# Kernel tuning notes

Hardware: AMD Instinct MI355X
Metric: run time of the kernel (lower is better)

Reference implementation:

```python
import jax, jax.numpy as jnp
import numpy as np

B = 1024      # graphs per batch
N = 64        # nodes per graph
DEG = 8       # edges per node
E = B * N * DEG
V = 52737     # vocab (different_ids)
D = 512       # embed / hidden dim
K1, K2, K3 = 52, 42, 34  # ceil(0.8*64), ceil(0.8*52), ceil(0.8*42)


def setup_inputs() -> dict:
    key = jax.random.key(0)
    ks = jax.random.split(key, 40)
    x_ids = jax.random.randint(ks[0], (B * N,), 0, V)
    off = jnp.repeat(jnp.arange(B) * N, N * DEG)  # graph offsets per edge
    edge_src = jax.random.randint(ks[1], (E,), 0, N) + off
    edge_dst = jax.random.randint(ks[2], (E,), 0, N) + off

    def lin(k, i, o):
        return jax.random.normal(k, (i, o), jnp.float32) / np.float32(np.sqrt(i))

    inp = dict(x_ids=x_ids, edge_src=edge_src, edge_dst=edge_dst)
    inp['emb'] = jax.random.normal(ks[3], (V, D), jnp.float32)
    # SAGEConv params: w*l/b*l act on aggregated neighbors, w*r on root
    for i, (kl, kr) in enumerate([(4, 5), (6, 7), (8, 9)], start=1):
        inp[f'w{i}l'] = lin(ks[kl], D, D)
        inp[f'b{i}l'] = jnp.zeros((D,), jnp.float32)
        inp[f'w{i}r'] = lin(ks[kr], D, D)
    # TopKPooling score vectors
    inp['p1'] = jax.random.normal(ks[10], (D,), jnp.float32)
    inp['p2'] = jax.random.normal(ks[11], (D,), jnp.float32)
    inp['p3'] = jax.random.normal(ks[12], (D,), jnp.float32)
    dims = [(1024, 512), (512, 256), (256, 128), (128, 64), (64, 1)]
    for i, (di, do) in enumerate(dims, start=1):
        inp[f'lw{i}'] = lin(ks[12 + i], di, do)
        inp[f'lb{i}'] = jnp.zeros((do,), jnp.float32)
    return inp


def _sage(x, src, dst, emask, wl, bl, wr):
    # PyG SAGEConv: mean-aggregate neighbor messages (src -> dst), plus root term
    n = x.shape[0]
    msg = x[src] * emask[:, None]
    s = jax.ops.segment_sum(msg, dst, num_segments=n)
    c = jax.ops.segment_sum(emask, dst, num_segments=n)
    agg = s / jnp.maximum(c, 1.0)[:, None]  # empty neighborhoods -> 0
    return agg @ wl + bl + x @ wr


def _topk_pool(x, src, dst, emask, w, k):
    # PyG TopKPooling: score = tanh(x.w / ||w||); keep top-k per graph, gate x
    n = x.shape[0]
    n_per = n // B
    score = jnp.tanh((x @ w) / jnp.linalg.norm(w))
    _, idx = jax.lax.top_k(score.reshape(B, n_per), k)      # [B, k] local ids
    perm = (idx + jnp.arange(B)[:, None] * n_per).reshape(-1)  # global ids
    x_new = x[perm] * score[perm][:, None]
    new_id = jnp.full((n,), -1, jnp.int32).at[perm].set(jnp.arange(B * k, dtype=jnp.int32))
    ns, nd = new_id[src], new_id[dst]
    valid = emask * (ns >= 0) * (nd >= 0)
    ns = jnp.where(valid > 0, ns, 0)
    nd = jnp.where(valid > 0, nd, 0)
    return x_new, ns, nd, valid.astype(x.dtype)


def _readout(x, k):
    xg = x.reshape(B, k, -1)
    return jnp.concatenate([xg.max(axis=1), xg.mean(axis=1)], axis=1)  # [B, 2F]


def _forward(x_ids, edge_src, edge_dst, emb,
             w1l, b1l, w1r, w2l, b2l, w2r, w3l, b3l, w3r,
             p1, p2, p3,
             lw1, lb1, lw2, lb2, lw3, lb3, lw4, lb4, lw5, lb5):
    x = emb[x_ids]                                  # [B*N, D]
    src, dst = edge_src, edge_dst
    emask = jnp.ones((E,), x.dtype)

    x = jax.nn.relu(_sage(x, src, dst, emask, w1l, b1l, w1r))
    x, src, dst, emask = _topk_pool(x, src, dst, emask, p1, K1)
    x1 = _readout(x, K1)

    x = jax.nn.relu(_sage(x, src, dst, emask, w2l, b2l, w2r))
    x, src, dst, emask = _topk_pool(x, src, dst, emask, p2, K2)
    x2 = _readout(x, K2)

    x = jax.nn.relu(_sage(x, src, dst, emask, w3l, b3l, w3r))
    x, src, dst, emask = _topk_pool(x, src, dst, emask, p3, K3)
    x3 = _readout(x, K3)

    h = x1 + x2 + x3                                # [B, 1024]
    h = jax.nn.relu(h @ lw1 + lb1)
    h = jax.nn.relu(h @ lw2 + lb2)
    h = jax.nn.relu(h @ lw3 + lb3)
    h = jax.nn.relu(h @ lw4 + lb4)
    # dropout p=0.5 is identity in eval mode
    return jax.nn.sigmoid(h @ lw5 + lb5)[:, 0]      # [B]


def reference(x_ids, edge_src, edge_dst, emb,
              w1l, b1l, w1r, w2l, b2l, w2r, w3l, b3l, w3r,
              p1, p2, p3,
              lw1, lb1, lw2, lb2, lw3, lb3, lw4, lb4, lw5, lb5):
    return _forward(x_ids, edge_src, edge_dst, emb,
                    w1l, b1l, w1r, w2l, b2l, w2r, w3l, b3l, w3r,
                    p1, p2, p3,
                    lw1, lb1, lw2, lb2, lw3, lb3, lw4, lb4, lw5, lb5)
```

## Files before the change

### kernel.cpp

```cpp
#include <hip/hip_runtime.h>
#include <math.h>

#define BG 1024
#define EPG 512
#define ETOT (BG*EPG)
#define DIM 512
#define KP1 52
#define KP2 42
#define KP3 34

typedef unsigned int uint;
typedef short s16x8 __attribute__((ext_vector_type(8)));
typedef float f32x4 __attribute__((ext_vector_type(4)));

__device__ __forceinline__ unsigned short f2b(float x) {
    uint u = __float_as_uint(x);
    u = u + 0x7fffu + ((u >> 16) & 1u);
    return (unsigned short)(u >> 16);
}
__device__ __forceinline__ float b2f(unsigned short h) {
    return __uint_as_float(((uint)h) << 16);
}
__device__ __forceinline__ void splitf(float x, unsigned short& h, unsigned short& l) {
    h = f2b(x);
    l = f2b(x - b2f(h));
}
__device__ __forceinline__ uint pk2(unsigned short a, unsigned short b) {
    return (uint)a | ((uint)b << 16);
}

__device__ __forceinline__ void gload16(const void* g, void* l) {
    __builtin_amdgcn_global_load_lds(
        (const __attribute__((address_space(1))) void*)g,
        (__attribute__((address_space(3))) void*)l, 16, 0, 0);
}

__global__ void __launch_bounds__(256)
gather_split(const int* __restrict__ ids, const float* __restrict__ emb,
             unsigned short* __restrict__ Xhi, unsigned short* __restrict__ Xlo)
{
    int tid = blockIdx.x * 256 + threadIdx.x;
    int row = tid >> 6;
    int c8  = (tid & 63) * 8;
    const float4* s = (const float4*)(emb + (size_t)ids[row] * DIM + c8);
    float4 v0 = s[0], v1 = s[1];
    float vs[8] = {v0.x,v0.y,v0.z,v0.w,v1.x,v1.y,v1.z,v1.w};
    unsigned short h[8], l[8];
#pragma unroll
    for (int i = 0; i < 8; ++i) splitf(vs[i], h[i], l[i]);
    uint4 H, L;
    H.x = pk2(h[0],h[1]); H.y = pk2(h[2],h[3]); H.z = pk2(h[4],h[5]); H.w = pk2(h[6],h[7]);
    L.x = pk2(l[0],l[1]); L.y = pk2(l[2],l[3]); L.z = pk2(l[4],l[5]); L.w = pk2(l[6],l[7]);
    *(uint4*)(Xhi + (size_t)row * DIM + c8) = H;
    *(uint4*)(Xlo + (size_t)row * DIM + c8) = L;
}

struct WPtrs { const float* w[6]; };

__global__ void __launch_bounds__(256)
split_wT_all(WPtrs p, unsigned short* __restrict__ WT)
{
    const int wi = blockIdx.x >> 8;
    const int bb = blockIdx.x & 255;
    const float* W = p.w[wi];
    unsigned short* Thi = WT + (size_t)(2 * wi) * DIM * DIM;
    unsigned short* Tlo = Thi + (size_t)DIM * DIM;
    __shared__ float tl[32][33];
    const int t  = threadIdx.x;
    const int bx = bb & 15;
    const int by = bb >> 4;
    const int lx = t & 31, ly = t >> 5;
    for (int r = ly; r < 32; r += 8)
        tl[r][lx] = W[(size_t)(by*32 + r) * DIM + bx*32 + lx];
    __syncthreads();
    for (int r = ly; r < 32; r += 8) {
        float v = tl[lx][r];
        unsigned short h, l; splitf(v, h, l);
        size_t o = (size_t)(bx*32 + r) * DIM + by*32 + lx;
        Thi[o] = h; Tlo[o] = l;
    }
}

template<int NPER>
__global__ void __launch_bounds__(256, 4)
agg_lds4(const unsigned short* __restrict__ Xhi, const unsigned short* __restrict__ Xlo,
         const int* __restrict__ esrc, const int* __restrict__ edst,
         const float* __restrict__ emask,
         unsigned short* __restrict__ Ghi, unsigned short* __restrict__ Glo)
{
    const int g  = blockIdx.x >> 2;
    const int c0 = (blockIdx.x & 3) * 128;
    const int t  = threadIdx.x;
    __shared__ __align__(16) unsigned short xs[NPER * 256];
    __shared__ int ldst[EPG];
    __shared__ int lsrc[EPG];
    __shared__ int ssrc[EPG];
    __shared__ int cnt4[4][64];
    __shared__ int offs[NPER + 1];

    for (int s = t; s < NPER * 32; s += 256) {
        const int row  = s >> 5;
        const int half = (s >> 4) & 1;
        const int c8   = (s & 15) * 8;
        const unsigned short* src =
            (half ? Xlo : Xhi) + (size_t)(g * NPER + row) * DIM + c0 + c8;
        gload16(src, (char*)xs + (size_t)s * 16);
    }
    const int eb = g * EPG;
    for (int e = t; e < EPG; e += 256) {
        float m = emask ? emask[eb + e] : 1.0f;
        ldst[e] = (m > 0.f) ? (edst[eb + e] - g * NPER) : -1;
        lsrc[e] = esrc[eb + e] - g * NPER;
    }
    __syncthreads();
    {
        const int d = t & 63, q = t >> 6;
        int c = 0;
        for (int e = q * 128; e < q * 128 + 128; ++e) c += (ldst[e] == d);
        cnt4[q][d] = c;
    }
    __syncthreads();
    if (t == 0) {
        int s = 0;
        for (int i = 0; i < NPER; ++i) {
            offs[i] = s;
            s += cnt4[0][i] + cnt4[1][i] + cnt4[2][i] + cnt4[3][i];
        }
        offs[NPER] = s;
    }
    __syncthreads();
    {
        const int d = t & 63, q = t >> 6;
        if (d < NPER) {
            int w = offs[d];
            for (int q2 = 0; q2 < q; ++q2) w += cnt4[q2][d];
            for (int e = q * 128; e < q * 128 + 128; ++e)
                if (ldst[e] == d) ssrc[w++] = lsrc[e];
        }
    }
    __syncthreads();
    const int ch = (t & 31) * 4;
    const int d0 = t >> 5;
    for (int d = d0; d < NPER; d += 8) {
        const int cA = offs[d], cB = offs[d + 1];
        float s0 = 0.f, s1 = 0.f, s2 = 0.f, s3 = 0.f;
        for (int j = cA; j < cB; ++j) {
            const int base = ssrc[j] * 256 + ch;
            ushort4 h = *(const ushort4*)&xs[base];
            ushort4 l = *(const ushort4*)&xs[base + 128];
            s0 += b2f(h.x) + b2f(l.x);
            s1 += b2f(h.y) + b2f(l.y);
            s2 += b2f(h.z) + b2f(l.z);
            s3 += b2f(h.w) + b2f(l.w);
        }
        const float den = fmaxf((float)(cB - cA), 1.0f);
        s0 /= den; s1 /= den; s2 /= den; s3 /= den;
        unsigned short h0,h1,h2,h3,l0,l1,l2,l3;
        splitf(s0,h0,l0); splitf(s1,h1,l1); splitf(s2,h2,l2); splitf(s3,h3,l3);
        const size_t wo = (size_t)(g * NPER + d) * DIM + c0 + ch;
        *(uint2*)(Ghi + wo) = make_uint2(pk2(h0,h1), pk2(h2,h3));
        *(uint2*)(Glo + wo) = make_uint2(pk2(l0,l1), pk2(l2,l3));
    }
}

__global__ void __launch_bounds__(256)
gemm_sage(const unsigned short* __restrict__ Ghi, const unsigned short* __restrict__ Glo,
          const unsigned short* __restrict__ WLhi, const unsigned short* __restrict__ WLlo,
          const unsigned short* __restrict__ Xhi, const unsigned short* __restrict__ Xlo,
          const unsigned short* __restrict__ WRhi, const unsigned short* __restrict__ WRlo,
          const float* __restrict__ bias, float* __restrict__ C, int M)
{
    __shared__ unsigned short sA[128 * 64];
    __shared__ unsigned short sW[128 * 64];

    const int t = threadIdx.x;
    const uint nwg = gridDim.x;
    const uint q8  = nwg >> 3;
    const uint bid = blockIdx.x;
    const uint sw  = (bid & 7) * q8 + (bid >> 3);
    const int  m0  = (int)(sw >> 2) * 128;
    const int  n0  = (int)(sw & 3) * 128;

    const int l  = t & 63;
    const int w  = t >> 6;
    const int wr = w >> 1;
    const int wc = w & 1;
    const int lr = l & 15;
    const int lq = l >> 4;

    f32x4 acc[4][4];
#pragma unroll
    for (int i = 0; i < 4; ++i)
#pragma unroll
        for (int j = 0; j < 4; ++j) acc[i][j] = (f32x4){0.f, 0.f, 0.f, 0.f};

    uint srow[4], soff[4];
#pragma unroll
    for (int i = 0; i < 4; ++i) {
        uint p = (uint)i * 256u + (uint)t;
        uint row = p >> 3, pc = p & 7;
        srow[i] = row;
        soff[i] = (pc ^ (row & 7u)) * 8u;
    }

#pragma unroll 1
    for (int s = 0; s < 6; ++s) {
        const int src = (s >= 3) ? 1 : 0;
        const int combo = s - src * 3;
        const unsigned short* Ap = src ? ((combo == 2) ? Xlo : Xhi)
                                       : ((combo == 2) ? Glo : Ghi);
        const unsigned short* Wp = src ? ((combo == 1) ? WRlo : WRhi)
                                       : ((combo == 1) ? WLlo : WLhi);
#pragma unroll 1
        for (int kt = 0; kt < 8; ++kt) {
            const int kb = kt * 64;
#pragma unroll
            for (int i = 0; i < 4; ++i) {
                const unsigned short* ga =
                    Ap + (size_t)(m0 + srow[i]) * DIM + kb + soff[i];
                const unsigned short* gw =
                    Wp + (size_t)(n0 + srow[i]) * DIM + kb + soff[i];
                uint p16 = ((uint)i * 256u + (uint)t) * 16u;
                gload16(ga, (char*)sA + p16);
                gload16(gw, (char*)sW + p16);
            }
            __syncthreads();
#pragma unroll
            for (int ks = 0; ks < 2; ++ks) {
                s16x8 af[4], wf[4];
#pragma unroll
                for (int i = 0; i < 4; ++i) {
                    int arow = wr * 64 + i * 16 + lr;
                    int off = arow * 128 + 16 * ((ks * 4 + lq) ^ (arow & 7));
                    af[i] = *(const s16x8*)((const char*)sA + off);
                }
#pragma unroll
                for (int j = 0; j < 4; ++j) {
                    int wrow = wc * 64 + j * 16 + lr;
                    int off = wrow * 128 + 16 * ((ks * 4 + lq) ^ (wrow & 7));
                    wf[j] = *(const s16x8*)((const char*)sW + off);
                }
#pragma unroll
                for (int i = 0; i < 4; ++i)
#pragma unroll
                    for (int j = 0; j < 4; ++j)
                        acc[i][j] = __builtin_amdgcn_mfma_f32_16x16x32_bf16(
                            af[i], wf[j], acc[i][j], 0, 0, 0);
            }
            __syncthreads();
        }
    }

#pragma unroll
    for (int i = 0; i < 4; ++i) {
        const int r0 = m0 + wr * 64 + i * 16 + lq * 4;
#pragma unroll
        for (int j = 0; j < 4; ++j) {
            const int cc = n0 + wc * 64 + j * 16 + lr;
            const float bv = bias[cc];
#pragma unroll
            for (int r = 0; r < 4; ++r) {
                float v = acc[i][j][r] + bv;
                C[(size_t)(r0 + r) * DIM + cc] = fmaxf(v, 0.f);
            }
        }
    }
}

template<int NPER, int KEEP>
__global__ void __launch_bounds__(256)
topk_split(const float* __restrict__ Y, const float* __restrict__ p,
           unsigned short* __restrict__ Xhi, unsigned short* __restrict__ Xlo,
           int* __restrict__ newid)
{
    const int g = blockIdx.x;
    const int t = threadIdx.x;
    const int wave = t >> 6, lane = t & 63;
    __shared__ float ssc[NPER];
    __shared__ float spnorm;
    __shared__ int   perm[KEEP];
    __shared__ float sgate[KEEP];

    if (wave == 0) {
        float v = 0.f;
#pragma unroll
        for (int i = 0; i < 8; ++i) { float x = p[lane + i * 64]; v = fmaf(x, x, v); }
#pragma unroll
        for (int off = 32; off; off >>= 1) v += __shfl_down(v, off);
        if (lane == 0) spnorm = sqrtf(v);
    }
    for (int nl = wave; nl < NPER; nl += 4) {
        const float* yr = Y + (size_t)(g * NPER + nl) * DIM;
        float v = 0.f;
#pragma unroll
        for (int i = 0; i < 8; ++i) v = fmaf(yr[lane + i * 64], p[lane + i * 64], v);
#pragma unroll
        for (int off = 32; off; off >>= 1) v += __shfl_down(v, off);
        if (lane == 0) ssc[nl] = v;
    }
    __syncthreads();
    float s = 0.f;
    if (t < NPER) s = tanhf(ssc[t] / spnorm);
    __syncthreads();
    if (t < NPER) ssc[t] = s;
    __syncthreads();
    if (t < NPER) {
        int r = 0;
        for (int j = 0; j < NPER; ++j) {
            float sj = ssc[j];
            r += (sj > s) || (sj == s && j < t);
        }
        newid[g * NPER + t] = (r < KEEP) ? (g * KEEP + r) : -1;
        if (r < KEEP) { perm[r] = t; sgate[r] = s; }
    }
    __syncthreads();
    for (int r = 0; r < KEEP; ++r) {
        const float2* src = (const float2*)(Y + (size_t)(g * NPER + perm[r]) * DIM);
        const float sv = sgate[r];
        float2 v = src[t];
        float a = v.x * sv, b = v.y * sv;
        unsigned short ha, la, hb, lb;
        splitf(a, ha, la); splitf(b, hb, lb);
        size_t o = (size_t)(g * KEEP + r) * DIM + 2 * t;
        *(uint*)(Xhi + o) = pk2(ha, hb);
        *(uint*)(Xlo + o) = pk2(la, lb);
    }
}

__global__ void __launch_bounds__(256)
remap_kernel(const int* __restrict__ es, const int* __restrict__ ed,
             const float* __restrict__ em, const int* __restrict__ newid,
             int* __restrict__ nes, int* __restrict__ ned, float* __restrict__ nem)
{
    int e = blockIdx.x * 256 + threadIdx.x;
    if (e >= ETOT) return;
    float m = em ? em[e] : 1.f;
    int s = newid[es[e]];
    int d = newid[ed[e]];
    bool v = (m > 0.f) && (s >= 0) && (d >= 0);
    nes[e] = v ? s : 0;
    ned[e] = v ? d : 0;
    nem[e] = v ? 1.f : 0.f;
}

__global__ void __launch_bounds__(256)
readout_split(const unsigned short* __restrict__ Xhi, const unsigned short* __restrict__ Xlo,
              float* __restrict__ H, int keep, int init)
{
    const int g = blockIdx.x;
    const int t = threadIdx.x;
    for (int c = t; c < DIM; c += 256) {
        float mx = -1e30f, sm = 0.f;
        for (int r = 0; r < keep; ++r) {
            size_t o = (size_t)(g * keep + r) * DIM + c;
            float v = b2f(Xhi[o]) + b2f(Xlo[o]);
            mx = fmaxf(mx, v); sm += v;
        }
        float mean = sm / (float)keep;
        size_t o = (size_t)g * 1024;
        if (init) { H[o + c] = mx;  H[o + 512 + c] = mean; }
        else      { H[o + c] += mx; H[o + 512 + c] += mean; }
    }
}

__global__ void __launch_bounds__(256)
mlp_fused(const float* __restrict__ H,
          const float* __restrict__ lw1, const float* __restrict__ lb1,
          const float* __restrict__ lw2, const float* __restrict__ lb2,
          const float* __restrict__ lw3, const float* __restrict__ lb3,
          const float* __restrict__ lw4, const float* __restrict__ lb4,
          const float* __restrict__ lw5, const float* __restrict__ lb5,
          float* __restrict__ out)
{
    __shared__ float h0[2][1024];
    __shared__ float y1[2][512];
    __shared__ float y2[2][256];
    __shared__ float y3[2][128];
    __shared__ float y4[2][64];
    const int t = threadIdx.x;
    const int r0 = blockIdx.x * 2;

    {
        float4 a = *(const float4*)&H[(size_t)r0 * 1024 + t * 4];
        float4 b = *(const float4*)&H[(size_t)(r0 + 1) * 1024 + t * 4];
        *(float4*)&h0[0][t * 4] = a;
        *(float4*)&h0[1][t * 4] = b;
    }
    __syncthreads();
    {
        float a00 = 0.f, a01 = 0.f, a10 = 0.f, a11 = 0.f;
        const int c = t * 2;
#pragma unroll 4
        for (int k = 0; k < 1024; ++k) {
            float2 wv = *(const float2*)&lw1[(size_t)k * 512 + c];
            float x0 = h0[0][k], x1 = h0[1][k];
            a00 = fmaf(x0, wv.x, a00); a01 = fmaf(x0, wv.y, a01);
            a10 = fmaf(x1, wv.x, a10); a11 = fmaf(x1, wv.y, a11);
        }
        y1[0][c]     = fmaxf(a00 + lb1[c], 0.f);
        y1[0][c + 1] = fmaxf(a01 + lb1[c + 1], 0.f);
        y1[1][c]     = fmaxf(a10 + lb1[c], 0.f);
        y1[1][c + 1] = fmaxf(a11 + lb1[c + 1], 0.f);
    }
    __syncthreads();
    {
        float a0 = 0.f, a1 = 0.f;
#pragma unroll 4
        for (int k = 0; k < 512; ++k) {
            float wv = lw2[(size_t)k * 256 + t];
            a0 = fmaf(y1[0][k], wv, a0);
            a1 = fmaf(y1[1][k], wv, a1);
        }
        y2[0][t] = fmaxf(a0 + lb2[t], 0.f);
        y2[1][t] = fmaxf(a1 + lb2[t], 0.f);
    }
    __syncthreads();
    if (t < 128) {
        float a0 = 0.f, a1 = 0.f;
#pragma unroll 4
        for (int k = 0; k < 256; ++k) {
            float wv = lw3[(size_t)k * 128 + t];
            a0 = fmaf(y2[0][k], wv, a0);
            a1 = fmaf(y2[1][k], wv, a1);
        }
        y3[0][t] = fmaxf(a0 + lb3[t], 0.f);
        y3[1][t] = fmaxf(a1 + lb3[t], 0.f);
    }
    __syncthreads();
    if (t < 64) {
        float a0 = 0.f, a1 = 0.f;
#pragma unroll 4
        for (int k = 0; k < 128; ++k) {
            float wv = lw4[(size_t)k * 64 + t];
            a0 = fmaf(y3[0][k], wv, a0);
            a1 = fmaf(y3[1][k], wv, a1);
        }
        y4[0][t] = fmaxf(a0 + lb4[t], 0.f);
        y4[1][t] = fmaxf(a1 + lb4[t], 0.f);
    }
    __syncthreads();
    const int wv = t >> 6, ln = t & 63;
    if (wv < 2) {
        float v = y4[wv][ln] * lw5[ln];
#pragma unroll
        for (int off = 32; off; off >>= 1) v += __shfl_down(v, off);
        if (ln == 0) out[r0 + wv] = 1.f / (1.f + expf(-(v + lb5[0])));
    }
}

extern "C" void kernel_launch(void* const* d_in, const int* in_sizes, int n_in,
                              void* d_out, int out_size, void* d_ws, size_t ws_size,
                              hipStream_t stream)
{
    const int*   x_ids = (const int*)d_in[0];
    const int*   esrc  = (const int*)d_in[1];
    const int*   edst  = (const int*)d_in[2];
    const float* emb   = (const float*)d_in[3];
    const float* w1l = (const float*)d_in[4],  *b1l = (const float*)d_in[5],  *w1r = (const float*)d_in[6];
    const float* w2l = (const float*)d_in[7],  *b2l = (const float*)d_in[8],  *w2r = (const float*)d_in[9];
    const float* w3l = (const float*)d_in[10], *b3l = (const float*)d_in[11], *w3r = (const float*)d_in[12];
    const float* p1  = (const float*)d_in[13];
    const float* p2  = (const float*)d_in[14];
    const float* p3  = (const float*)d_in[15];
    const float* lw1 = (const float*)d_in[16], *lb1 = (const float*)d_in[17];
    const float* lw2 = (const float*)d_in[18], *lb2 = (const float*)d_in[19];
    const float* lw3 = (const float*)d_in[20], *lb3 = (const float*)d_in[21];
    const float* lw4 = (const float*)d_in[22], *lb4 = (const float*)d_in[23];
    const float* lw5 = (const float*)d_in[24], *lb5 = (const float*)d_in[25];
    float* out = (float*)d_out;

    const size_t PL = (size_t)65536 * DIM;
    unsigned short* Xhi = (unsigned short*)d_ws;
    unsigned short* Xlo = Xhi + PL;
    unsigned short* Ghi = Xlo + PL;
    unsigned short* Glo = Ghi + PL;
    float* Cc = (float*)(Glo + PL);
    float* H  = Cc + PL;
    int* newid = (int*)(H + (size_t)1024 * 1024);
    int*   ES2 = newid + 65536;
    int*   ED2 = ES2 + ETOT;
    float* EM2 = (float*)(ED2 + ETOT);
    int*   ES3 = (int*)(EM2 + ETOT);
    int*   ED3 = ES3 + ETOT;
    float* EM3 = (float*)(ED3 + ETOT);
    unsigned short* WT = (unsigned short*)(EM3 + ETOT);
    const size_t WSZ = (size_t)DIM * DIM;
    unsigned short *w1lh = WT + 0*WSZ,  *w1ll = WT + 1*WSZ;
    unsigned short *w1rh = WT + 2*WSZ,  *w1rl = WT + 3*WSZ;
    unsigned short *w2lh = WT + 4*WSZ,  *w2ll = WT + 5*WSZ;
    unsigned short *w2rh = WT + 6*WSZ,  *w2rl = WT + 7*WSZ;
    unsigned short *w3lh = WT + 8*WSZ,  *w3ll = WT + 9*WSZ;
    unsigned short *w3rh = WT + 10*WSZ, *w3rl = WT + 11*WSZ;

    WPtrs wp;
    wp.w[0] = w1l; wp.w[1] = w1r; wp.w[2] = w2l;
    wp.w[3] = w2r; wp.w[4] = w3l; wp.w[5] = w3r;
    split_wT_all<<<6 * 256, 256, 0, stream>>>(wp, WT);

    gather_split<<<16384, 256, 0, stream>>>(x_ids, emb, Xhi, Xlo);
    agg_lds4<64><<<BG * 4, 256, 0, stream>>>(Xhi, Xlo, esrc, edst, nullptr, Ghi, Glo);
    gemm_sage<<<(65536/128)*4, 256, 0, stream>>>(Ghi, Glo, w1lh, w1ll,
                                                 Xhi, Xlo, w1rh, w1rl, b1l, Cc, 65536);
    topk_split<64, KP1><<<BG, 256, 0, stream>>>(Cc, p1, Xhi, Xlo, newid);
    remap_kernel<<<ETOT/256, 256, 0, stream>>>(esrc, edst, nullptr, newid, ES2, ED2, EM2);
    readout_split<<<BG, 256, 0, stream>>>(Xhi, Xlo, H, KP1, 1);

    agg_lds4<KP1><<<BG * 4, 256, 0, stream>>>(Xhi, Xlo, ES2, ED2, EM2, Ghi, Glo);
    gemm_sage<<<(53248/128)*4, 256, 0, stream>>>(Ghi, Glo, w2lh, w2ll,
                                                 Xhi, Xlo, w2rh, w2rl, b2l, Cc, 53248);
    topk_split<KP1, KP2><<<BG, 256, 0, stream>>>(Cc, p2, Xhi, Xlo, newid);
    remap_kernel<<<ETOT/256, 256, 0, stream>>>(ES2, ED2, EM2, newid, ES3, ED3, EM3);
    readout_split<<<BG, 256, 0, stream>>>(Xhi, Xlo, H, KP2, 0);

    agg_lds4<KP2><<<BG * 4, 256, 0, stream>>>(Xhi, Xlo, ES3, ED3, EM3, Ghi, Glo);
    gemm_sage<<<(43008/128)*4, 256, 0, stream>>>(Ghi, Glo, w3lh, w3ll,
                                                 Xhi, Xlo, w3rh, w3rl, b3l, Cc, 43008);
    topk_split<KP2, KP3><<<BG, 256, 0, stream>>>(Cc, p3, Xhi, Xlo, newid);
    readout_split<<<BG, 256, 0, stream>>>(Xhi, Xlo, H, KP3, 0);

    mlp_fused<<<512, 256, 0, stream>>>(H, lw1, lb1, lw2, lb2, lw3, lb3,
                                       lw4, lb4, lw5, lb5, out);
}
```

Before: 1.389 ms.

## Use 256x256 double-buffered 8-wave GEMM for SAGE layers

Replaces the 128x128, 4-wave SAGE GEMM with a 256x256-tile, 512-thread kernel. The new kernel double-buffers LDS and prefetches the next k-slice while the current one runs MFMAs. All six hi/lo split segments are flattened into one 48-step k loop, and MFMA phases are interleaved with barriers and setprio. The aim is to hide global-load latency and raise operand reuse per tile. The cost is 128KB of LDS and fewer workgroups, which lowers occupancy and gives a poorer tail for the smaller M values (43008 is not divisible by 256*8 swizzle groups, so risk there).

```diff
diff --git a/kernel.cpp b/kernel.cpp
--- a/kernel.cpp
+++ b/kernel.cpp
@@ -163,97 +163,122 @@
     }
 }
 
-__global__ void __launch_bounds__(256)
-gemm_sage(const unsigned short* __restrict__ Ghi, const unsigned short* __restrict__ Glo,
-          const unsigned short* __restrict__ WLhi, const unsigned short* __restrict__ WLlo,
-          const unsigned short* __restrict__ Xhi, const unsigned short* __restrict__ Xlo,
-          const unsigned short* __restrict__ WRhi, const unsigned short* __restrict__ WRlo,
-          const float* __restrict__ bias, float* __restrict__ C, int M)
-{
-    __shared__ unsigned short sA[128 * 64];
-    __shared__ unsigned short sW[128 * 64];
+__global__ void __launch_bounds__(512)
+gemm_sage8(const unsigned short* __restrict__ Ghi, const unsigned short* __restrict__ Glo,
+           const unsigned short* __restrict__ WLhi, const unsigned short* __restrict__ WLlo,
+           const unsigned short* __restrict__ Xhi, const unsigned short* __restrict__ Xlo,
+           const unsigned short* __restrict__ WRhi, const unsigned short* __restrict__ WRlo,
+           const float* __restrict__ bias, float* __restrict__ C, int M)
+{
+    __shared__ unsigned short sA[2][256 * 64];
+    __shared__ unsigned short sW[2][256 * 64];
 
     const int t = threadIdx.x;
     const uint nwg = gridDim.x;
     const uint q8  = nwg >> 3;
     const uint bid = blockIdx.x;
     const uint sw  = (bid & 7) * q8 + (bid >> 3);
-    const int  m0  = (int)(sw >> 2) * 128;
-    const int  n0  = (int)(sw & 3) * 128;
+    const int  m0  = (int)(sw >> 1) * 256;
+    const int  n0  = (int)(sw & 1) * 256;
 
     const int l  = t & 63;
     const int w  = t >> 6;
-    const int wr = w >> 1;
-    const int wc = w & 1;
+    const int wr = w >> 2;
+    const int wc = w & 3;
     const int lr = l & 15;
     const int lq = l >> 4;
 
-    f32x4 acc[4][4];
-#pragma unroll
-    for (int i = 0; i < 4; ++i)
+    f32x4 acc[8][4];
+#pragma unroll
+    for (int i = 0; i < 8; ++i)
 #pragma unroll
         for (int j = 0; j < 4; ++j) acc[i][j] = (f32x4){0.f, 0.f, 0.f, 0.f};
 
     uint srow[4], soff[4];
 #pragma unroll
     for (int i = 0; i < 4; ++i) {
-        uint p = (uint)i * 256u + (uint)t;
-        uint row = p >> 3, pc = p & 7;
-        srow[i] = row;
-        soff[i] = (pc ^ (row & 7u)) * 8u;
-    }
+        uint p = (uint)i * 512u + (uint)t;
+        srow[i] = p >> 3;
+        soff[i] = ((p & 7u) ^ (srow[i] & 7u)) * 8u;
+    }
+
+    const unsigned short* Aseg;
+    const unsigned short* Wseg;
+    int kb;
+#define SEGSEL(kt)                                                     \
+    {   int s_ = (kt) >> 3; kb = ((kt) & 7) << 6;                      \
+        if      (s_ == 0) { Aseg = Ghi; Wseg = WLhi; }                 \
+        else if (s_ == 1) { Aseg = Ghi; Wseg = WLlo; }                 \
+        else if (s_ == 2) { Aseg = Glo; Wseg = WLhi; }                 \
+        else if (s_ == 3) { Aseg = Xhi; Wseg = WRhi; }                 \
+        else if (s_ == 4) { Aseg = Xhi; Wseg = WRlo; }                 \
+        else              { Aseg = Xlo; Wseg = WRhi; } }
+
+#define STAGE(dst)                                                     \
+    _Pragma("unroll")                                                  \
+    for (int i = 0; i < 4; ++i) {                                      \
+        const unsigned short* ga =                                     \
+            Aseg + (size_t)(m0 + (int)srow[i]) * DIM + kb + soff[i];   \
+        const unsigned short* gw =                                     \
+            Wseg + (size_t)(n0 + (int)srow[i]) * DIM + kb + soff[i];   \
+        uint p16 = ((uint)i * 512u + (uint)t) * 16u;                   \
+        gload16(ga, (char*)sA[dst] + p16);                             \
+        gload16(gw, (char*)sW[dst] + p16);                             \
+    }
+
+    SEGSEL(0);
+    STAGE(0);
+    int cur = 0;
 
 #pragma unroll 1
-    for (int s = 0; s < 6; ++s) {
-        const int src = (s >= 3) ? 1 : 0;
-        const int combo = s - src * 3;
-        const unsigned short* Ap = src ? ((combo == 2) ? Xlo : Xhi)
-                                       : ((combo == 2) ? Glo : Ghi);
-        const unsigned short* Wp = src ? ((combo == 1) ? WRlo : WRhi)
-                                       : ((combo == 1) ? WLlo : WLhi);
-#pragma unroll 1
-        for (int kt = 0; kt < 8; ++kt) {
-            const int kb = kt * 64;
-#pragma unroll
-            for (int i = 0; i < 4; ++i) {
-                const unsigned short* ga =
-                    Ap + (size_t)(m0 + srow[i]) * DIM + kb + soff[i];
-                const unsigned short* gw =
-                    Wp + (size_t)(n0 + srow[i]) * DIM + kb + soff[i];
-                uint p16 = ((uint)i * 256u + (uint)t) * 16u;
-                gload16(ga, (char*)sA + p16);
-                gload16(gw, (char*)sW + p16);
+    for (int kt = 0; kt < 48; ++kt) {
+        asm volatile("s_waitcnt vmcnt(0)" ::: "memory");
+        __syncthreads();
+        if (kt < 47) {
+            SEGSEL(kt + 1);
+            STAGE(cur ^ 1);
+        }
+        __builtin_amdgcn_sched_barrier(0);
+        const char* la = (const char*)sA[cur];
+        const char* lw = (const char*)sW[cur];
+#pragma unroll
+        for (int p = 0; p < 4; ++p) {
+            const int ks = p >> 1;
+            const int mh = p & 1;
+            s16x8 af[4], wf[4];
+#pragma unroll
+            for (int i2 = 0; i2 < 4; ++i2) {
+                int arow = wr * 128 + (mh * 4 + i2) * 16 + lr;
+                int off  = arow * 128 + 16 * ((ks * 4 + lq) ^ (arow & 7));
+                af[i2] = *(const s16x8*)(la + off);
             }
+#pragma unroll
+            for (int j = 0; j < 4; ++j) {
+                int wrow = wc * 64 + j * 16 + lr;
+                int off  = wrow * 128 + 16 * ((ks * 4 + lq) ^ (wrow & 7));
+                wf[j] = *(const s16x8*)(lw + off);
+            }
+            __builtin_amdgcn_sched_barrier(0);
             __syncthreads();
-#pragma unroll
-            for (int ks = 0; ks < 2; ++ks) {
-                s16x8 af[4], wf[4];
-#pragma unroll
-                for (int i = 0; i < 4; ++i) {
-                    int arow = wr * 64 + i * 16 + lr;
-                    int off = arow * 128 + 16 * ((ks * 4 + lq) ^ (arow & 7));
-                    af[i] = *(const s16x8*)((const char*)sA + off);
-                }
-#pragma unroll
-                for (int j = 0; j < 4; ++j) {
-                    int wrow = wc * 64 + j * 16 + lr;
-                    int off = wrow * 128 + 16 * ((ks * 4 + lq) ^ (wrow & 7));
-                    wf[j] = *(const s16x8*)((const char*)sW + off);
-                }
-#pragma unroll
-                for (int i = 0; i < 4; ++i)
-#pragma unroll
-                    for (int j = 0; j < 4; ++j)
-                        acc[i][j] = __builtin_amdgcn_mfma_f32_16x16x32_bf16(
-                            af[i], wf[j], acc[i][j], 0, 0, 0);
-            }
+            __builtin_amdgcn_s_setprio(1);
+#pragma unroll
+            for (int i2 = 0; i2 < 4; ++i2)
+#pragma unroll
+                for (int j = 0; j < 4; ++j)
+                    acc[mh * 4 + i2][j] = __builtin_amdgcn_mfma_f32_16x16x32_bf16(
+                        af[i2], wf[j], acc[mh * 4 + i2][j], 0, 0, 0);
+            __builtin_amdgcn_s_setprio(0);
+            __builtin_amdgcn_sched_barrier(0);
             __syncthreads();
         }
-    }
-
-#pragma unroll
-    for (int i = 0; i < 4; ++i) {
-        const int r0 = m0 + wr * 64 + i * 16 + lq * 4;
+        cur ^= 1;
+    }
+#undef STAGE
+#undef SEGSEL
+
+#pragma unroll
+    for (int i = 0; i < 8; ++i) {
+        const int r0 = m0 + wr * 128 + i * 16 + lq * 4;
 #pragma unroll
         for (int j = 0; j < 4; ++j) {
             const int cc = n0 + wc * 64 + j * 16 + lr;
@@ -499,22 +524,22 @@
 
     gather_split<<<16384, 256, 0, stream>>>(x_ids, emb, Xhi, Xlo);
     agg_lds4<64><<<BG * 4, 256, 0, stream>>>(Xhi, Xlo, esrc, edst, nullptr, Ghi, Glo);
-    gemm_sage<<<(65536/128)*4, 256, 0, stream>>>(Ghi, Glo, w1lh, w1ll,
-                                                 Xhi, Xlo, w1rh, w1rl, b1l, Cc, 65536);
+    gemm_sage8<<<(65536/256)*2, 512, 0, stream>>>(Ghi, Glo, w1lh, w1ll,
+                                                  Xhi, Xlo, w1rh, w1rl, b1l, Cc, 65536);
     topk_split<64, KP1><<<BG, 256, 0, stream>>>(Cc, p1, Xhi, Xlo, newid);
     remap_kernel<<<ETOT/256, 256, 0, stream>>>(esrc, edst, nullptr, newid, ES2, ED2, EM2);
     readout_split<<<BG, 256, 0, stream>>>(Xhi, Xlo, H, KP1, 1);
 
     agg_lds4<KP1><<<BG * 4, 256, 0, stream>>>(Xhi, Xlo, ES2, ED2, EM2, Ghi, Glo);
-    gemm_sage<<<(53248/128)*4, 256, 0, stream>>>(Ghi, Glo, w2lh, w2ll,
-                                                 Xhi, Xlo, w2rh, w2rl, b2l, Cc, 53248);
+    gemm_sage8<<<(53248/256)*2, 512, 0, stream>>>(Ghi, Glo, w2lh, w2ll,
+                                                  Xhi, Xlo, w2rh, w2rl, b2l, Cc, 53248);
     topk_split<KP1, KP2><<<BG, 256, 0, stream>>>(Cc, p2, Xhi, Xlo, newid);
     remap_kernel<<<ETOT/256, 256, 0, stream>>>(ES2, ED2, EM2, newid, ES3, ED3, EM3);
     readout_split<<<BG, 256, 0, stream>>>(Xhi, Xlo, H, KP2, 0);
 
     agg_lds4<KP2><<<BG * 4, 256, 0, stream>>>(Xhi, Xlo, ES3, ED3, EM3, Ghi, Glo);
-    gemm_sage<<<(43008/128)*4, 256, 0, stream>>>(Ghi, Glo, w3lh, w3ll,
-                                                 Xhi, Xlo, w3rh, w3rl, b3l, Cc, 43008);
+    gemm_sage8<<<(43008/256)*2, 512, 0, stream>>>(Ghi, Glo, w3lh, w3ll,
+                                                  Xhi, Xlo, w3rh, w3rl, b3l, Cc, 43008);
     topk_split<KP2, KP3><<<BG, 256, 0, stream>>>(Cc, p3, Xhi, Xlo, newid);
     readout_split<<<BG, 256, 0, stream>>>(Xhi, Xlo, H, KP3, 0);
 
```

Measured after the change: 1.685 ms. 1.21x slower.

## Fuse top-k pooling, edge remap and readout into one per-graph kernel

Applied to the files above, without the earlier changes.

The top-k selection kernel now also computes the max/mean readout from the gated values it already holds in registers, and remaps that graph's edges using a shared-memory newid table. This drops two kernel launches per pooling stage, the global newid buffer, and the readout's re-read of the split hi/lo node features. In exchange the per-graph block does more serial work, and readout now uses the unsplit fp32 values instead of the hi+lo reconstruction, which can differ slightly. The remap assumes edge sources and destinations stay inside their own graph.

```diff
diff --git a/kernel.cpp b/kernel.cpp
--- a/kernel.cpp
+++ b/kernel.cpp
@@ -267,11 +267,14 @@
     }
 }
 
-template<int NPER, int KEEP>
+template<int NPER, int KEEP, bool REMAP, bool INIT>
 __global__ void __launch_bounds__(256)
-topk_split(const float* __restrict__ Y, const float* __restrict__ p,
+pool_fused(const float* __restrict__ Y, const float* __restrict__ p,
            unsigned short* __restrict__ Xhi, unsigned short* __restrict__ Xlo,
-           int* __restrict__ newid)
+           const int* __restrict__ es, const int* __restrict__ ed,
+           const float* __restrict__ em,
+           int* __restrict__ nes, int* __restrict__ ned, float* __restrict__ nem,
+           float* __restrict__ H)
 {
     const int g = blockIdx.x;
     const int t = threadIdx.x;
@@ -280,6 +283,7 @@
     __shared__ float spnorm;
     __shared__ int   perm[KEEP];
     __shared__ float sgate[KEEP];
+    __shared__ int   lnewid[NPER];
 
     if (wave == 0) {
         float v = 0.f;
@@ -310,56 +314,50 @@
             float sj = ssc[j];
             r += (sj > s) || (sj == s && j < t);
         }
-        newid[g * NPER + t] = (r < KEEP) ? (g * KEEP + r) : -1;
+        lnewid[t] = (r < KEEP) ? (g * KEEP + r) : -1;
         if (r < KEEP) { perm[r] = t; sgate[r] = s; }
     }
     __syncthreads();
+
+    float mx0 = -1e30f, mx1 = -1e30f, sm0 = 0.f, sm1 = 0.f;
     for (int r = 0; r < KEEP; ++r) {
-        const float2* src = (const float2*)(Y + (size_t)(g * NPER + perm[r]) * DIM);
+        const float2 v = ((const float2*)(Y + (size_t)(g * NPER + perm[r]) * DIM))[t];
         const float sv = sgate[r];
-        float2 v = src[t];
         float a = v.x * sv, b = v.y * sv;
+        mx0 = fmaxf(mx0, a); mx1 = fmaxf(mx1, b);
+        sm0 += a; sm1 += b;
         unsigned short ha, la, hb, lb;
         splitf(a, ha, la); splitf(b, hb, lb);
         size_t o = (size_t)(g * KEEP + r) * DIM + 2 * t;
         *(uint*)(Xhi + o) = pk2(ha, hb);
         *(uint*)(Xlo + o) = pk2(la, lb);
     }
-}
-
-__global__ void __launch_bounds__(256)
-remap_kernel(const int* __restrict__ es, const int* __restrict__ ed,
-             const float* __restrict__ em, const int* __restrict__ newid,
-             int* __restrict__ nes, int* __restrict__ ned, float* __restrict__ nem)
-{
-    int e = blockIdx.x * 256 + threadIdx.x;
-    if (e >= ETOT) return;
-    float m = em ? em[e] : 1.f;
-    int s = newid[es[e]];
-    int d = newid[ed[e]];
-    bool v = (m > 0.f) && (s >= 0) && (d >= 0);
-    nes[e] = v ? s : 0;
-    ned[e] = v ? d : 0;
-    nem[e] = v ? 1.f : 0.f;
-}
-
-__global__ void __launch_bounds__(256)
-readout_split(const unsigned short* __restrict__ Xhi, const unsigned short* __restrict__ Xlo,
-              float* __restrict__ H, int keep, int init)
-{
-    const int g = blockIdx.x;
-    const int t = threadIdx.x;
-    for (int c = t; c < DIM; c += 256) {
-        float mx = -1e30f, sm = 0.f;
-        for (int r = 0; r < keep; ++r) {
-            size_t o = (size_t)(g * keep + r) * DIM + c;
-            float v = b2f(Xhi[o]) + b2f(Xlo[o]);
-            mx = fmaxf(mx, v); sm += v;
-        }
-        float mean = sm / (float)keep;
-        size_t o = (size_t)g * 1024;
-        if (init) { H[o + c] = mx;  H[o + 512 + c] = mean; }
-        else      { H[o + c] += mx; H[o + 512 + c] += mean; }
+    {
+        const size_t o = (size_t)g * 1024;
+        const float me0 = sm0 / (float)KEEP, me1 = sm1 / (float)KEEP;
+        if (INIT) {
+            H[o + 2*t]       = mx0; H[o + 2*t + 1]       = mx1;
+            H[o + 512 + 2*t] = me0; H[o + 512 + 2*t + 1] = me1;
+        } else {
+            H[o + 2*t]       += mx0; H[o + 2*t + 1]       += mx1;
+            H[o + 512 + 2*t] += me0; H[o + 512 + 2*t + 1] += me1;
+        }
+    }
+
+    if (REMAP) {
+        const int eb = g * EPG;
+        for (int e = t; e < EPG; e += 256) {
+            const float m = em ? em[eb + e] : 1.f;
+            int sN = -1, dN = -1;
+            if (m > 0.f) {
+                sN = lnewid[es[eb + e] - g * NPER];
+                dN = lnewid[ed[eb + e] - g * NPER];
+            }
+            const bool v = (m > 0.f) && (sN >= 0) && (dN >= 0);
+            nes[eb + e] = v ? sN : 0;
+            ned[eb + e] = v ? dN : 0;
+            nem[eb + e] = v ? 1.f : 0.f;
+        }
     }
 }
 
@@ -476,8 +474,7 @@
     unsigned short* Glo = Ghi + PL;
     float* Cc = (float*)(Glo + PL);
     float* H  = Cc + PL;
-    int* newid = (int*)(H + (size_t)1024 * 1024);
-    int*   ES2 = newid + 65536;
+    int*   ES2 = (int*)(H + (size_t)1024 * 1024);
     int*   ED2 = ES2 + ETOT;
     float* EM2 = (float*)(ED2 + ETOT);
     int*   ES3 = (int*)(EM2 + ETOT);
@@ -501,22 +498,20 @@
     agg_lds4<64><<<BG * 4, 256, 0, stream>>>(Xhi, Xlo, esrc, edst, nullptr, Ghi, Glo);
     gemm_sage<<<(65536/128)*4, 256, 0, stream>>>(Ghi, Glo, w1lh, w1ll,
                                                  Xhi, Xlo, w1rh, w1rl, b1l, Cc, 65536);
-    topk_split<64, KP1><<<BG, 256, 0, stream>>>(Cc, p1, Xhi, Xlo, newid);
-    remap_kernel<<<ETOT/256, 256, 0, stream>>>(esrc, edst, nullptr, newid, ES2, ED2, EM2);
-    readout_split<<<BG, 256, 0, stream>>>(Xhi, Xlo, H, KP1, 1);
+    pool_fused<64, KP1, true, true><<<BG, 256, 0, stream>>>(
+        Cc, p1, Xhi, Xlo, esrc, edst, nullptr, ES2, ED2, EM2, H);
 
     agg_lds4<KP1><<<BG * 4, 256, 0, stream>>>(Xhi, Xlo, ES2, ED2, EM2, Ghi, Glo);
     gemm_sage<<<(53248/128)*4, 256, 0, stream>>>(Ghi, Glo, w2lh, w2ll,
                                                  Xhi, Xlo, w2rh, w2rl, b2l, Cc, 53248);
-    topk_split<KP1, KP2><<<BG, 256, 0, stream>>>(Cc, p2, Xhi, Xlo, newid);
-    remap_kernel<<<ETOT/256, 256, 0, stream>>>(ES2, ED2, EM2, newid, ES3, ED3, EM3);
-    readout_split<<<BG, 256, 0, stream>>>(Xhi, Xlo, H, KP2, 0);
+    pool_fused<KP1, KP2, true, false><<<BG, 256, 0, stream>>>(
+        Cc, p2, Xhi, Xlo, ES2, ED2, EM2, ES3, ED3, EM3, H);
 
     agg_lds4<KP2><<<BG * 4, 256, 0, stream>>>(Xhi, Xlo, ES3, ED3, EM3, Ghi, Glo);
     gemm_sage<<<(43008/128)*4, 256, 0, stream>>>(Ghi, Glo, w3lh, w3ll,
                                                  Xhi, Xlo, w3rh, w3rl, b3l, Cc, 43008);
-    topk_split<KP2, KP3><<<BG, 256, 0, stream>>>(Cc, p3, Xhi, Xlo, newid);
-    readout_split<<<BG, 256, 0, stream>>>(Xhi, Xlo, H, KP3, 0);
+    pool_fused<KP2, KP3, false, false><<<BG, 256, 0, stream>>>(
+        Cc, p3, Xhi, Xlo, nullptr, nullptr, nullptr, nullptr, nullptr, nullptr, H);
 
     mlp_fused<<<512, 256, 0, stream>>>(H, lw1, lb1, lw2, lb2, lw3, lb3,
                                        lw4, lb4, lw5, lb5, out);
```

After: 1.306 ms. -6.0%, faster.
